# Performance work log

Hardware: AMD Instinct MI355X
Metric: run time of the kernel (lower is better)

The kernel has to match this reference:

```python
import jax, jax.numpy as jnp
import numpy as np

ALPHA = 0.2  # LeakyReLU negative slope


def setup_inputs() -> dict:
    key = jax.random.key(0)
    k1, k2, k3, k4 = jax.random.split(key, 4)
    B, N, F_IN, F_OUT = 4, 4096, 256, 256
    h = jax.random.normal(k1, (B, N, F_IN), dtype=jnp.float32)
    adj = jax.random.randint(k2, (B, N, N), 0, 2, dtype=jnp.int32)
    # xavier_normal with gain=1.414: std = gain*sqrt(2/(fan_in+fan_out))
    std_W = 1.414 * np.sqrt(2.0 / (F_IN + F_OUT))
    W = jax.random.normal(k3, (F_IN, F_OUT), dtype=jnp.float32) * std_W
    std_a = 1.414 * np.sqrt(2.0 / (1 + 2 * F_OUT))
    a = jax.random.normal(k4, (1, 2 * F_OUT), dtype=jnp.float32) * std_a
    return {"h": h, "adj": adj, "W": W, "a": a}


def reference(h, adj, W, a):
    # h: [B, N, F_in], adj: [B, N, N] (0/1), W: [F_in, F_out], a: [1, 2*F_out]
    F_out = W.shape[1]
    Hh = jnp.einsum('bni,io->bno', h, W)               # [B, N, F_out]
    a_src = a[0, :F_out]                                # attends to edge source i
    a_dst = a[0, F_out:]                                # attends to edge target j
    s = jnp.einsum('bno,o->bn', Hh, a_src)              # [B, N]
    d = jnp.einsum('bno,o->bn', Hh, a_dst)              # [B, N]
    # score(i,j) = a . concat(Hh_i, Hh_j) = s_i + d_j
    logits = s[:, :, None] + d[:, None, :]              # [B, N, N]
    # edge_e = exp(-leakyrelu(score)) only on edges (adj nonzero), else 0
    e = jnp.where(adj != 0,
                  jnp.exp(-jax.nn.leaky_relu(logits, negative_slope=ALPHA)),
                  jnp.zeros((), dtype=Hh.dtype))        # [B, N, N]
    rowsum = jnp.sum(e, axis=-1, keepdims=True)         # [B, N, 1]
    # rows with zero sum keep divisor 1 (as in the torch code)
    rowsum = jnp.where(rowsum == 0.0, 1.0, rowsum)
    h_prime = jnp.einsum('bnm,bmo->bno', e, Hh) / rowsum  # [B, N, F_out]
    return jax.nn.elu(h_prime)  # concat=True branch
```

## Files before the change

kernel.cpp:

```cpp
#include <hip/hip_runtime.h>

#define LRELU_ALPHA 0.2f

typedef __bf16 bf16x8 __attribute__((ext_vector_type(8)));
typedef unsigned short u16;
typedef unsigned short u16x8 __attribute__((ext_vector_type(8)));
typedef float f32x4 __attribute__((ext_vector_type(4)));
typedef int int4v __attribute__((ext_vector_type(4)));

__device__ __forceinline__ u16 f2bf(float f) {
  unsigned int u = __float_as_uint(f);
  u += 0x7fffu + ((u >> 16) & 1u);
  return (u16)(u >> 16);
}

__device__ __forceinline__ void gload16(const void* g, void* lds) {
  __builtin_amdgcn_global_load_lds(
      (const __attribute__((address_space(1))) void*)g,
      (__attribute__((address_space(3))) void*)lds, 16, 0, 0);
}

__global__ __launch_bounds__(256) void wcast(const float* __restrict__ W,
                                             u16* __restrict__ WbT) {
  int idx = blockIdx.x * 256 + threadIdx.x;
  WbT[idx] = f2bf(W[(idx & 255) * 256 + (idx >> 8)]);
}

__global__ __launch_bounds__(256) void gemm1(const float* __restrict__ h,
                                             const u16* __restrict__ WbT,
                                             const float* __restrict__ a,
                                             u16* __restrict__ HhT,
                                             float* __restrict__ sbuf,
                                             float* __restrict__ dbuf) {
  const int tid = threadIdx.x, bid = blockIdx.x;
  const int l = tid & 63, w = tid >> 6;
  const int lr = l & 15;
  const int lk = (l >> 4) << 3;
  const int rowA = bid * 64 + 16 * w + lr;
  const float* hrow = h + (size_t)rowA * 256 + lk;

  f32x4 acc[16];
#pragma unroll
  for (int n = 0; n < 16; ++n) acc[n] = (f32x4){0.f, 0.f, 0.f, 0.f};

  for (int k0 = 0; k0 < 256; k0 += 32) {
    f32x4 a0 = *(const f32x4*)(hrow + k0);
    f32x4 a1 = *(const f32x4*)(hrow + k0 + 4);
    u16x8 au;
    au[0] = f2bf(a0[0]); au[1] = f2bf(a0[1]); au[2] = f2bf(a0[2]); au[3] = f2bf(a0[3]);
    au[4] = f2bf(a1[0]); au[5] = f2bf(a1[1]); au[6] = f2bf(a1[2]); au[7] = f2bf(a1[3]);
    bf16x8 af = __builtin_bit_cast(bf16x8, au);
#pragma unroll
    for (int n = 0; n < 16; ++n) {
      int4v bv = *(const int4v*)(WbT + (size_t)(16 * n + lr) * 256 + k0 + lk);
      bf16x8 bf = __builtin_bit_cast(bf16x8, bv);
      acc[n] = __builtin_amdgcn_mfma_f32_16x16x32_bf16(af, bf, acc[n], 0, 0, 0);
    }
  }

  float sp[4] = {0.f, 0.f, 0.f, 0.f}, dp[4] = {0.f, 0.f, 0.f, 0.f};
#pragma unroll
  for (int n = 0; n < 16; ++n) {
    int col = 16 * n + lr;
    float as = a[col];
    float ad = a[256 + col];
#pragma unroll
    for (int rr = 0; rr < 4; ++rr) {
      int row = bid * 64 + 16 * w + ((l >> 4) << 2) + rr;
      int bb = row >> 12, nl = row & 4095;
      float v = acc[n][rr];
      HhT[((size_t)(bb * 256 + col)) * 4096 + nl] = f2bf(v);
      sp[rr] += v * as;
      dp[rr] += v * ad;
    }
  }
#pragma unroll
  for (int rr = 0; rr < 4; ++rr) {
#pragma unroll
    for (int off = 1; off < 16; off <<= 1) {
      sp[rr] += __shfl_xor(sp[rr], off);
      dp[rr] += __shfl_xor(dp[rr], off);
    }
  }
  if ((l & 15) == 0) {
#pragma unroll
    for (int rr = 0; rr < 4; ++rr) {
      int row = bid * 64 + 16 * w + ((l >> 4) << 2) + rr;
      sbuf[row] = sp[rr];
      dbuf[row] = dp[rr];
    }
  }
}

__global__ __launch_bounds__(512, 2) void gat_main(const int* __restrict__ adj,
                                                   const u16* __restrict__ HhT,
                                                   const float* __restrict__ s,
                                                   const float* __restrict__ d,
                                                   float* __restrict__ out) {
  __shared__ __align__(16) u16 Bt4[4][8192];
  __shared__ __align__(16) int At4[4][2048];
  __shared__ __align__(16) float Dt4[4][32];
  __shared__ float rs_lds[64];

  const int tid = threadIdx.x, bid = blockIdx.x;
  const int xcd = bid & 7;
  const int t256 = (xcd << 5) | (bid >> 3);
  const int b = t256 >> 6;
  const int rowbase = (t256 & 63) << 6;

  const int l = tid & 63, w = tid >> 6;
  const int wr = w & 3, wc = w >> 2;
  const int lr = l & 15, lkg = l >> 4;
  const int rowt = 16 * wr + lr;
  const float s_row = s[b * 4096 + rowbase + rowt];

  const char* HhTb = (const char*)HhT + (size_t)b * 2097152;
  const int csB = (l & 3) ^ ((l >> 3) & 3);
  const char* bsrc0 = HhTb + (size_t)(w * 32 +      (l >> 2)) * 8192 + csB * 16;
  const char* bsrc1 = HhTb + (size_t)(w * 32 + 16 + (l >> 2)) * 8192 + csB * 16;
  const int csA = (l & 7) ^ (l >> 3);
  const char* asrc = (const char*)adj +
      ((size_t)(b * 4096 + rowbase + w * 8 + (l >> 3))) * 16384 + csA * 16;
  const char* dsrc = (const char*)d + (size_t)b * 16384 + w * 16;

  char* BtB = (char*)&Bt4[0][0];
  char* AtB = (char*)&At4[0][0];
  char* DtB = (char*)&Dt4[0][0];

  const int atoff0 = rowt * 128 + (((2 * lkg)     ^ (lr & 7)) * 16);
  const int atoff1 = rowt * 128 + (((2 * lkg + 1) ^ (lr & 7)) * 16);
  const int btbase = (128 * wc + lr) * 64 + ((lkg ^ ((lr >> 1) & 3)) * 16);
  const int dtoff = lkg * 32;

  f32x4 acc[8];
#pragma unroll
  for (int n = 0; n < 8; ++n) acc[n] = (f32x4){0.f, 0.f, 0.f, 0.f};
  float racc = 0.f;

#define ISSUE(NXT, STEP)                                                      \
  {                                                                           \
    const size_t st_ = (size_t)(STEP);                                        \
    gload16(bsrc0 + st_ * 64,  BtB + (NXT) * 16384 + (w * 2 + 0) * 1024);     \
    gload16(bsrc1 + st_ * 64,  BtB + (NXT) * 16384 + (w * 2 + 1) * 1024);     \
    gload16(asrc + st_ * 128,  AtB + (NXT) * 8192 + w * 1024);                \
    if (l == 0) gload16(dsrc + st_ * 128, DtB + (NXT) * 128 + w * 16);        \
  }

#define COMPUTE(CUR)                                                          \
  {                                                                           \
    int4v aA = *(const int4v*)(AtB + (CUR) * 8192 + atoff0);                  \
    int4v aB = *(const int4v*)(AtB + (CUR) * 8192 + atoff1);                  \
    f32x4 dA = *(const f32x4*)(DtB + (CUR) * 128 + dtoff);                    \
    f32x4 dB = *(const f32x4*)(DtB + (CUR) * 128 + dtoff + 16);               \
    u16x8 au_;                                                                \
    {                                                                         \
      int aj[8] = {aA.x, aA.y, aA.z, aA.w, aB.x, aB.y, aB.z, aB.w};           \
      float dv[8] = {dA[0], dA[1], dA[2], dA[3], dB[0], dB[1], dB[2], dB[3]}; \
      _Pragma("unroll")                                                       \
      for (int j = 0; j < 8; ++j) {                                           \
        float lg = s_row + dv[j];                                             \
        float t = fmaxf(lg, LRELU_ALPHA * lg);                                \
        float e = (aj[j] != 0) ? __expf(-t) : 0.f;                            \
        racc += e;                                                            \
        au_[j] = f2bf(e);                                                     \
      }                                                                       \
    }                                                                         \
    bf16x8 af = __builtin_bit_cast(bf16x8, au_);                              \
    __builtin_amdgcn_s_setprio(1);                                            \
    _Pragma("unroll")                                                         \
    for (int n = 0; n < 8; ++n) {                                             \
      bf16x8 bfv = __builtin_bit_cast(bf16x8,                                 \
          *(const int4v*)(BtB + (CUR) * 16384 + btbase + n * 1024));          \
      acc[n] = __builtin_amdgcn_mfma_f32_16x16x32_bf16(af, bfv, acc[n],       \
                                                       0, 0, 0);              \
    }                                                                         \
    __builtin_amdgcn_s_setprio(0);                                            \
  }

#define WAITS(VN)                                                             \
    asm volatile("s_waitcnt lgkmcnt(0)" ::: "memory");                        \
    asm volatile("s_waitcnt vmcnt(" #VN ")" ::: "memory");                    \
    __builtin_amdgcn_s_barrier();

  ISSUE(0, 0)
  ISSUE(1, 1)
  ISSUE(2, 2)
  asm volatile("s_waitcnt vmcnt(8)" ::: "memory");
  __builtin_amdgcn_s_barrier();

  for (int k = 0; k < 124; k += 4) {
    ISSUE(3, k + 3) COMPUTE(0) WAITS(8)
    ISSUE(0, k + 4) COMPUTE(1) WAITS(8)
    ISSUE(1, k + 5) COMPUTE(2) WAITS(8)
    ISSUE(2, k + 6) COMPUTE(3) WAITS(8)
  }
  ISSUE(3, 127) COMPUTE(0) WAITS(8)
  COMPUTE(1) WAITS(4)
  COMPUTE(2) WAITS(0)
  COMPUTE(3)
#undef ISSUE
#undef COMPUTE
#undef WAITS

  racc += __shfl_xor(racc, 16);
  racc += __shfl_xor(racc, 32);
  if (wc == 0 && l < 16) rs_lds[16 * wr + l] = (racc == 0.f) ? 1.f : racc;
  __syncthreads();

#pragma unroll
  for (int rr = 0; rr < 4; ++rr) {
    int rin = 16 * wr + (lkg << 2) + rr;
    float inv = 1.f / rs_lds[rin];
    size_t obase = ((size_t)(b * 4096 + rowbase + rin)) * 256 + 128 * wc;
#pragma unroll
    for (int n = 0; n < 8; ++n) {
      float v = acc[n][rr] * inv;
      out[obase + 16 * n + lr] = v > 0.f ? v : (__expf(v) - 1.f);
    }
  }
}

extern "C" void kernel_launch(void* const* d_in, const int* in_sizes, int n_in,
                              void* d_out, int out_size, void* d_ws, size_t ws_size,
                              hipStream_t stream) {
  const float* h = (const float*)d_in[0];
  const int* adj = (const int*)d_in[1];
  const float* W = (const float*)d_in[2];
  const float* a = (const float*)d_in[3];
  float* out = (float*)d_out;

  u16* WbT  = (u16*)d_ws;
  u16* HhT  = (u16*)((char*)d_ws + 131072);
  float* sb = (float*)((char*)d_ws + 131072 + 8388608);
  float* db = sb + 16384;

  hipLaunchKernelGGL(wcast,    dim3(256), dim3(256), 0, stream, W, WbT);
  hipLaunchKernelGGL(gemm1,    dim3(256), dim3(256), 0, stream, h, WbT, a, HhT, sb, db);
  hipLaunchKernelGGL(gat_main, dim3(256), dim3(512), 0, stream, adj, HhT, sb, db, out);
}
```

Before: 176.2 us.

## Pack adjacency into bitmasks and decouple edge-weight generation from MFMA loop

A new packadj kernel compresses the int32 adjacency into 1-bit masks. gat_main then loads each block's mask rows and the full d vector into LDS up front. Edge weights are generated cooperatively per 32-column step into a double-buffered LDS tile, while HhT is stored in a tiled layout so B loads become contiguous. This trims the main kernel's per-step global traffic and the redundant exp work across waves. In exchange it adds a separate pass that still reads the full 256MB adjacency, plus extra LDS round-trips.

```diff
diff --git a/kernel.cpp b/kernel.cpp
--- a/kernel.cpp
+++ b/kernel.cpp
@@ -4,9 +4,11 @@
 
 typedef __bf16 bf16x8 __attribute__((ext_vector_type(8)));
 typedef unsigned short u16;
+typedef unsigned short u16x4v __attribute__((ext_vector_type(4)));
 typedef unsigned short u16x8 __attribute__((ext_vector_type(8)));
 typedef float f32x4 __attribute__((ext_vector_type(4)));
 typedef int int4v __attribute__((ext_vector_type(4)));
+typedef unsigned int u32;
 
 __device__ __forceinline__ u16 f2bf(float f) {
   unsigned int u = __float_as_uint(f);
@@ -26,10 +28,38 @@
   WbT[idx] = f2bf(W[(idx & 255) * 256 + (idx >> 8)]);
 }
 
+__global__ __launch_bounds__(256) void packadj(const int* __restrict__ adj,
+                                               u32* __restrict__ maskg) {
+  __shared__ unsigned char nib[1024];
+  const int tid = threadIdx.x;
+  const size_t row0 = (size_t)blockIdx.x * 8;
+  for (int rr = 0; rr < 8; ++rr) {
+    const size_t row = row0 + rr;
+    const int* arow = adj + row * 4096;
+    for (int it = 0; it < 4; ++it) {
+      int4v v = *(const int4v*)(arow + it * 1024 + tid * 4);
+      unsigned char nb = (unsigned char)((v.x != 0) | ((v.y != 0) << 1) |
+                                         ((v.z != 0) << 2) | ((v.w != 0) << 3));
+      nib[tid] = nb;
+      __syncthreads();
+      if (tid < 32) {
+        const u32* nw = (const u32*)nib;
+        u32 w0 = nw[tid * 2], w1 = nw[tid * 2 + 1];
+        u32 m = (w0 & 0xFu) | ((w0 >> 4) & 0xF0u) | ((w0 >> 8) & 0xF00u) |
+                ((w0 >> 12) & 0xF000u);
+        m |= ((w1 & 0xFu) | ((w1 >> 4) & 0xF0u) | ((w1 >> 8) & 0xF00u) |
+              ((w1 >> 12) & 0xF000u)) << 16;
+        maskg[row * 128 + it * 32 + tid] = m;
+      }
+      __syncthreads();
+    }
+  }
+}
+
 __global__ __launch_bounds__(256) void gemm1(const float* __restrict__ h,
                                              const u16* __restrict__ WbT,
                                              const float* __restrict__ a,
-                                             u16* __restrict__ HhT,
+                                             u16* __restrict__ HhTt,
                                              float* __restrict__ sbuf,
                                              float* __restrict__ dbuf) {
   const int tid = threadIdx.x, bid = blockIdx.x;
@@ -67,9 +97,12 @@
 #pragma unroll
     for (int rr = 0; rr < 4; ++rr) {
       int row = bid * 64 + 16 * w + ((l >> 4) << 2) + rr;
-      int bb = row >> 12, nl = row & 4095;
+      int bb = row >> 12, kk = row & 4095;
       float v = acc[n][rr];
-      HhT[((size_t)(bb * 256 + col)) * 4096 + nl] = f2bf(v);
+      size_t addr = (size_t)bb * 1048576 + (size_t)(kk >> 5) * 8192 +
+                    (col >> 4) * 512 + ((kk >> 3) & 3) * 128 + (col & 15) * 8 +
+                    (kk & 7);
+      HhTt[addr] = f2bf(v);
       sp[rr] += v * as;
       dp[rr] += v * ad;
     }
@@ -92,14 +125,15 @@
   }
 }
 
-__global__ __launch_bounds__(512, 2) void gat_main(const int* __restrict__ adj,
-                                                   const u16* __restrict__ HhT,
+__global__ __launch_bounds__(512, 2) void gat_main(const u32* __restrict__ maskg,
+                                                   const u16* __restrict__ HhTt,
                                                    const float* __restrict__ s,
                                                    const float* __restrict__ d,
                                                    float* __restrict__ out) {
-  __shared__ __align__(16) u16 Bt4[4][8192];
-  __shared__ __align__(16) int At4[4][2048];
-  __shared__ __align__(16) float Dt4[4][32];
+  __shared__ __align__(16) u16 Bt[4][8192];
+  __shared__ __align__(16) u16 At[2][2048];
+  __shared__ __align__(16) u32 Mk[8192];
+  __shared__ __align__(16) float Dl[4096];
   __shared__ float rs_lds[64];
 
   const int tid = threadIdx.x, bid = blockIdx.x;
@@ -109,72 +143,82 @@
   const int rowbase = (t256 & 63) << 6;
 
   const int l = tid & 63, w = tid >> 6;
-  const int wr = w & 3, wc = w >> 2;
   const int lr = l & 15, lkg = l >> 4;
-  const int rowt = 16 * wr + lr;
-  const float s_row = s[b * 4096 + rowbase + rowt];
-
-  const char* HhTb = (const char*)HhT + (size_t)b * 2097152;
-  const int csB = (l & 3) ^ ((l >> 3) & 3);
-  const char* bsrc0 = HhTb + (size_t)(w * 32 +      (l >> 2)) * 8192 + csB * 16;
-  const char* bsrc1 = HhTb + (size_t)(w * 32 + 16 + (l >> 2)) * 8192 + csB * 16;
-  const int csA = (l & 7) ^ (l >> 3);
-  const char* asrc = (const char*)adj +
-      ((size_t)(b * 4096 + rowbase + w * 8 + (l >> 3))) * 16384 + csA * 16;
-  const char* dsrc = (const char*)d + (size_t)b * 16384 + w * 16;
-
-  char* BtB = (char*)&Bt4[0][0];
-  char* AtB = (char*)&At4[0][0];
-  char* DtB = (char*)&Dt4[0][0];
-
-  const int atoff0 = rowt * 128 + (((2 * lkg)     ^ (lr & 7)) * 16);
-  const int atoff1 = rowt * 128 + (((2 * lkg + 1) ^ (lr & 7)) * 16);
-  const int btbase = (128 * wc + lr) * 64 + ((lkg ^ ((lr >> 1) & 3)) * 16);
-  const int dtoff = lkg * 32;
-
-  f32x4 acc[8];
-#pragma unroll
-  for (int n = 0; n < 8; ++n) acc[n] = (f32x4){0.f, 0.f, 0.f, 0.f};
+  const int wr = w & 1, wc = w >> 1;
+
+  for (int i = tid; i < 1024; i += 512)
+    *(f32x4*)&Dl[i * 4] = *(const f32x4*)(d + b * 4096 + i * 4);
+  {
+    const u32* mrow = maskg + (size_t)(b * 4096 + rowbase) * 128;
+    int r = tid >> 3, w0 = (tid & 7) * 16;
+#pragma unroll
+    for (int j = 0; j < 16; ++j) {
+      int ww = w0 + j;
+      Mk[r * 128 + ((ww + r) & 127)] = mrow[r * 128 + ww];
+    }
+  }
+
+  const int er = tid >> 3, c8 = tid & 7;
+  const float s_e = s[b * 4096 + rowbase + er];
+
+  const char* bsrc0 = (const char*)HhTt +
+      ((size_t)b * 1048576 + (2 * w + 0) * 512 + l * 8) * 2;
+  const char* bsrc1 = (const char*)HhTt +
+      ((size_t)b * 1048576 + (2 * w + 1) * 512 + l * 8) * 2;
+  char* BtB = (char*)&Bt[0][0];
+
+  const int atoff0 = (32 * wr + lr) * 32 + lkg * 8;
+  const int atoff1 = (32 * wr + 16 + lr) * 32 + lkg * 8;
+  const int btoff = 4 * wc * 512 + lkg * 128 + lr * 8;
+
+  f32x4 acc0[4], acc1[4];
+#pragma unroll
+  for (int n = 0; n < 4; ++n) {
+    acc0[n] = (f32x4){0.f, 0.f, 0.f, 0.f};
+    acc1[n] = (f32x4){0.f, 0.f, 0.f, 0.f};
+  }
   float racc = 0.f;
 
-#define ISSUE(NXT, STEP)                                                      \
+#define ISSUE(BUF, STEP)                                                      \
   {                                                                           \
-    const size_t st_ = (size_t)(STEP);                                        \
-    gload16(bsrc0 + st_ * 64,  BtB + (NXT) * 16384 + (w * 2 + 0) * 1024);     \
-    gload16(bsrc1 + st_ * 64,  BtB + (NXT) * 16384 + (w * 2 + 1) * 1024);     \
-    gload16(asrc + st_ * 128,  AtB + (NXT) * 8192 + w * 1024);                \
-    if (l == 0) gload16(dsrc + st_ * 128, DtB + (NXT) * 128 + w * 16);        \
-  }
-
-#define COMPUTE(CUR)                                                          \
+    const size_t so_ = (size_t)(STEP) * 16384;                                \
+    gload16(bsrc0 + so_, BtB + (BUF) * 16384 + (2 * w + 0) * 1024);           \
+    gload16(bsrc1 + so_, BtB + (BUF) * 16384 + (2 * w + 1) * 1024);           \
+  }
+
+#define EGEN(BUFA, STEP)                                                      \
   {                                                                           \
-    int4v aA = *(const int4v*)(AtB + (CUR) * 8192 + atoff0);                  \
-    int4v aB = *(const int4v*)(AtB + (CUR) * 8192 + atoff1);                  \
-    f32x4 dA = *(const f32x4*)(DtB + (CUR) * 128 + dtoff);                    \
-    f32x4 dB = *(const f32x4*)(DtB + (CUR) * 128 + dtoff + 16);               \
-    u16x8 au_;                                                                \
-    {                                                                         \
-      int aj[8] = {aA.x, aA.y, aA.z, aA.w, aB.x, aB.y, aB.z, aB.w};           \
-      float dv[8] = {dA[0], dA[1], dA[2], dA[3], dB[0], dB[1], dB[2], dB[3]}; \
-      _Pragma("unroll")                                                       \
-      for (int j = 0; j < 8; ++j) {                                           \
-        float lg = s_row + dv[j];                                             \
-        float t = fmaxf(lg, LRELU_ALPHA * lg);                                \
-        float e = (aj[j] != 0) ? __expf(-t) : 0.f;                            \
-        racc += e;                                                            \
-        au_[j] = f2bf(e);                                                     \
-      }                                                                       \
+    const int st_ = (STEP);                                                   \
+    u32 mword = Mk[er * 128 + ((st_ + er) & 127)];                            \
+    u32 m8 = mword >> (c8 * 4);                                               \
+    f32x4 dv = *(const f32x4*)&Dl[st_ * 32 + c8 * 4];                         \
+    u16x4v ev;                                                                \
+    _Pragma("unroll")                                                         \
+    for (int j = 0; j < 4; ++j) {                                             \
+      float lg = s_e + dv[j];                                                 \
+      float t = fmaxf(lg, LRELU_ALPHA * lg);                                  \
+      float e = ((m8 >> j) & 1) ? __expf(-t) : 0.f;                           \
+      racc += e;                                                              \
+      ev[j] = f2bf(e);                                                        \
     }                                                                         \
-    bf16x8 af = __builtin_bit_cast(bf16x8, au_);                              \
-    __builtin_amdgcn_s_setprio(1);                                            \
+    *(u16x4v*)&At[BUFA][er * 32 + c8 * 4] = ev;                               \
+  }
+
+#define COMPUTE(BUFB, BUFA)                                                   \
+  {                                                                           \
+    bf16x8 af0 = __builtin_bit_cast(bf16x8,                                   \
+        *(const int4v*)&At[BUFA][atoff0]);                                    \
+    bf16x8 af1 = __builtin_bit_cast(bf16x8,                                   \
+        *(const int4v*)&At[BUFA][atoff1]);                                    \
     _Pragma("unroll")                                                         \
-    for (int n = 0; n < 8; ++n) {                                             \
+    for (int n = 0; n < 4; ++n) {                                             \
       bf16x8 bfv = __builtin_bit_cast(bf16x8,                                 \
-          *(const int4v*)(BtB + (CUR) * 16384 + btbase + n * 1024));          \
-      acc[n] = __builtin_amdgcn_mfma_f32_16x16x32_bf16(af, bfv, acc[n],       \
-                                                       0, 0, 0);              \
+          *(const int4v*)&Bt[BUFB][btoff + n * 512]);                         \
+      acc0[n] = __builtin_amdgcn_mfma_f32_16x16x32_bf16(af0, bfv, acc0[n],    \
+                                                        0, 0, 0);             \
+      acc1[n] = __builtin_amdgcn_mfma_f32_16x16x32_bf16(af1, bfv, acc1[n],    \
+                                                        0, 0, 0);             \
     }                                                                         \
-    __builtin_amdgcn_s_setprio(0);                                            \
   }
 
 #define WAITS(VN)                                                             \
@@ -185,37 +229,44 @@
   ISSUE(0, 0)
   ISSUE(1, 1)
   ISSUE(2, 2)
-  asm volatile("s_waitcnt vmcnt(8)" ::: "memory");
+  __syncthreads();
+  EGEN(0, 0)
+  asm volatile("s_waitcnt lgkmcnt(0)" ::: "memory");
   __builtin_amdgcn_s_barrier();
 
   for (int k = 0; k < 124; k += 4) {
-    ISSUE(3, k + 3) COMPUTE(0) WAITS(8)
-    ISSUE(0, k + 4) COMPUTE(1) WAITS(8)
-    ISSUE(1, k + 5) COMPUTE(2) WAITS(8)
-    ISSUE(2, k + 6) COMPUTE(3) WAITS(8)
-  }
-  ISSUE(3, 127) COMPUTE(0) WAITS(8)
-  COMPUTE(1) WAITS(4)
-  COMPUTE(2) WAITS(0)
-  COMPUTE(3)
+    ISSUE(3, k + 3) EGEN(1, k + 1) COMPUTE(0, 0) WAITS(4)
+    ISSUE(0, k + 4) EGEN(0, k + 2) COMPUTE(1, 1) WAITS(4)
+    ISSUE(1, k + 5) EGEN(1, k + 3) COMPUTE(2, 0) WAITS(4)
+    ISSUE(2, k + 6) EGEN(0, k + 4) COMPUTE(3, 1) WAITS(4)
+  }
+  ISSUE(3, 127) EGEN(1, 125) COMPUTE(0, 0) WAITS(4)
+  EGEN(0, 126) COMPUTE(1, 1) WAITS(2)
+  EGEN(1, 127) COMPUTE(2, 0) WAITS(0)
+  COMPUTE(3, 1)
 #undef ISSUE
+#undef EGEN
 #undef COMPUTE
 #undef WAITS
 
-  racc += __shfl_xor(racc, 16);
-  racc += __shfl_xor(racc, 32);
-  if (wc == 0 && l < 16) rs_lds[16 * wr + l] = (racc == 0.f) ? 1.f : racc;
+  racc += __shfl_xor(racc, 1);
+  racc += __shfl_xor(racc, 2);
+  racc += __shfl_xor(racc, 4);
+  if (c8 == 0) rs_lds[er] = (racc == 0.f) ? 1.f : racc;
   __syncthreads();
 
 #pragma unroll
-  for (int rr = 0; rr < 4; ++rr) {
-    int rin = 16 * wr + (lkg << 2) + rr;
-    float inv = 1.f / rs_lds[rin];
-    size_t obase = ((size_t)(b * 4096 + rowbase + rin)) * 256 + 128 * wc;
-#pragma unroll
-    for (int n = 0; n < 8; ++n) {
-      float v = acc[n][rr] * inv;
-      out[obase + 16 * n + lr] = v > 0.f ? v : (__expf(v) - 1.f);
+  for (int t16 = 0; t16 < 2; ++t16) {
+#pragma unroll
+    for (int n = 0; n < 4; ++n) {
+#pragma unroll
+      for (int reg = 0; reg < 4; ++reg) {
+        int rloc = 32 * wr + 16 * t16 + lkg * 4 + reg;
+        int col = 64 * wc + 16 * n + lr;
+        float v = (t16 ? acc1[n][reg] : acc0[n][reg]) / rs_lds[rloc];
+        out[((size_t)(b * 4096 + rowbase + rloc)) * 256 + col] =
+            v > 0.f ? v : (__expf(v) - 1.f);
+      }
     }
   }
 }
@@ -229,12 +280,14 @@
   const float* a = (const float*)d_in[3];
   float* out = (float*)d_out;
 
-  u16* WbT  = (u16*)d_ws;
-  u16* HhT  = (u16*)((char*)d_ws + 131072);
-  float* sb = (float*)((char*)d_ws + 131072 + 8388608);
-  float* db = sb + 16384;
-
-  hipLaunchKernelGGL(wcast,    dim3(256), dim3(256), 0, stream, W, WbT);
-  hipLaunchKernelGGL(gemm1,    dim3(256), dim3(256), 0, stream, h, WbT, a, HhT, sb, db);
-  hipLaunchKernelGGL(gat_main, dim3(256), dim3(512), 0, stream, adj, HhT, sb, db, out);
-}
+  u16* WbT   = (u16*)d_ws;
+  u16* HhTt  = (u16*)((char*)d_ws + 131072);
+  float* sb  = (float*)((char*)d_ws + 131072 + 8388608);
+  float* db  = sb + 16384;
+  u32* maskg = (u32*)((char*)d_ws + 131072 + 8388608 + 131072);
+
+  hipLaunchKernelGGL(wcast,    dim3(256),  dim3(256), 0, stream, W, WbT);
+  hipLaunchKernelGGL(packadj,  dim3(2048), dim3(256), 0, stream, adj, maskg);
+  hipLaunchKernelGGL(gemm1,    dim3(256),  dim3(256), 0, stream, h, WbT, a, HhTt, sb, db);
+  hipLaunchKernelGGL(gat_main, dim3(256),  dim3(512), 0, stream, maskg, HhTt, sb, db, out);
+}
```

Result: faster. 165.8 us (-5.9%).
